# Optimization experiments

Measured on AMD Instinct MI355X. Metric: run time of the kernel, lower is better.

The kernel has to match this reference:

```python
import jax, jax.numpy as jnp
import numpy as np

NUM_HEADS = 16
THETA = 10000.0


def _rope(x, cos, sin):
    # x: [B, H, S, d_k]; cos/sin: [S, d_k//2] broadcast over B, H
    x1 = x[..., 0::2]
    x2 = x[..., 1::2]
    r1 = cos * x1 - sin * x2
    r2 = sin * x1 + cos * x2
    # interleave back: (..., half_d, 2) -> (..., d_k)
    return jnp.stack((r1, r2), axis=-1).reshape(x.shape)


def setup_inputs() -> dict:
    key = jax.random.key(0)
    ks = jax.random.split(key, 5)
    B, S, D = 4, 2048, 1024
    scale = D ** -0.5
    x = jax.random.normal(ks[0], (B, S, D), dtype=jnp.float32)
    wq = jax.random.normal(ks[1], (D, D), dtype=jnp.float32) * scale
    wk = jax.random.normal(ks[2], (D, D), dtype=jnp.float32) * scale
    wv = jax.random.normal(ks[3], (D, D), dtype=jnp.float32) * scale
    wo = jax.random.normal(ks[4], (D, D), dtype=jnp.float32) * scale
    return {"x": x, "wq": wq, "wk": wk, "wv": wv, "wo": wo}


def reference(x, wq, wk, wv, wo):
    B, S, D = x.shape
    H = NUM_HEADS
    dk = D // H

    def proj(w):
        # x @ w.T, split heads -> [B, H, S, dk]
        y = jnp.einsum('bsd,ed->bse', x, w)
        return y.reshape(B, S, H, dk).transpose(0, 2, 1, 3)

    q, k, v = proj(wq), proj(wk), proj(wv)

    # RoPE (interleaved pairs), positions = arange(S)
    inv_freq = THETA ** (-(jnp.arange(0, dk, 2, dtype=jnp.float32) / dk))
    ang = jnp.arange(S, dtype=jnp.float32)[:, None] * inv_freq  # [S, dk//2]
    cos, sin = jnp.cos(ang), jnp.sin(ang)
    q = _rope(q, cos, sin)
    k = _rope(k, cos, sin)

    scores = jnp.einsum('bhqd,bhkd->bhqk', q, k) / jnp.sqrt(jnp.asarray(dk, x.dtype))
    causal = jnp.tril(jnp.ones((S, S), dtype=bool))  # keep self + past
    scores = jnp.where(causal, scores, -jnp.inf)
    p = jax.nn.softmax(scores, axis=-1)
    attn = jnp.einsum('bhqk,bhkd->bhqd', p, v)
    attn = attn.transpose(0, 2, 1, 3).reshape(B, S, D)
    return jnp.einsum('bsd,ed->bse', attn, wo)
```

## Files before the change

### kernel.cpp

```cpp
#include <hip/hip_runtime.h>
#include <hip/hip_bf16.h>
#include <cstdint>
#include <cstddef>

#define Bb 4
#define Ss 2048
#define Dd 1024
#define Hh 16
#define Mm (Bb*Ss)

typedef __bf16 bf16_t;
typedef __bf16 bf16x8 __attribute__((ext_vector_type(8)));
typedef __bf16 bf16x4 __attribute__((ext_vector_type(4)));
typedef float  f32x4  __attribute__((ext_vector_type(4)));
typedef float  f32x16 __attribute__((ext_vector_type(16)));
typedef unsigned int u32x4 __attribute__((ext_vector_type(4)));
typedef unsigned int u32x2 __attribute__((ext_vector_type(2)));

#define MFMA16(a,b,c) __builtin_amdgcn_mfma_f32_16x16x32_bf16(a,b,c,0,0,0)
#define MFMA32(a,b,c) __builtin_amdgcn_mfma_f32_32x32x16_bf16(a,b,c,0,0,0)

#define QSCALE 0.18033688011112042f

static __device__ __forceinline__ float fexp2(float x) {
#if __has_builtin(__builtin_amdgcn_exp2f)
  return __builtin_amdgcn_exp2f(x);
#else
  return exp2f(x);
#endif
}

static __device__ __forceinline__ bf16x8 ld16g(const bf16_t* p) {
  return __builtin_bit_cast(bf16x8, *reinterpret_cast<const u32x4*>(p));
}

static __device__ __forceinline__ void gload_lds16(const bf16_t* g, bf16_t* l) {
  __builtin_amdgcn_global_load_lds(
      (__attribute__((address_space(1))) void*)(g),
      (__attribute__((address_space(3))) void*)(l),
      16, 0, 0);
}

__global__ void cvt_f32_bf16(const float* __restrict__ in, bf16_t* __restrict__ out) {
  int i = (blockIdx.x * blockDim.x + threadIdx.x) * 4;
  float4 f = *reinterpret_cast<const float4*>(in + i);
  out[i + 0] = (bf16_t)f.x;
  out[i + 1] = (bf16_t)f.y;
  out[i + 2] = (bf16_t)f.z;
  out[i + 3] = (bf16_t)f.w;
}

__global__ void cvt_w4(const float* __restrict__ w0, const float* __restrict__ w1,
                       const float* __restrict__ w2, const float* __restrict__ w3,
                       bf16_t* __restrict__ out) {
  int bid = blockIdx.x;
  int seg = bid >> 10, local = bid & 1023;
  const float* w = (seg == 0) ? w0 : (seg == 1) ? w1 : (seg == 2) ? w2 : w3;
  int i = (local * 256 + threadIdx.x) * 4;
  float4 f = *reinterpret_cast<const float4*>(w + i);
  bf16_t* o = out + (size_t)seg * (Dd * Dd) + i;
  o[0] = (bf16_t)f.x; o[1] = (bf16_t)f.y; o[2] = (bf16_t)f.z; o[3] = (bf16_t)f.w;
}

__global__ void rope_tab_k(float2* __restrict__ tab) {
  int idx = blockIdx.x * 256 + threadIdx.x;
  int i = idx & 31, s = idx >> 5;
  float inv_freq = exp2f(-(float)i * (13.2877123795494f / 32.0f));
  float ang = (float)s * inv_freq;
  float sn, cs;
  sincosf(ang, &sn, &cs);
  tab[idx] = make_float2(cs, sn);
}

template <typename OutT>
__global__ __launch_bounds__(256, 3) void gemm_r3(const bf16_t* __restrict__ A,
                                                  const bf16_t* __restrict__ Bm,
                                                  OutT* __restrict__ C0,
                                                  OutT* __restrict__ C1,
                                                  OutT* __restrict__ C2,
                                                  const float2* __restrict__ tab,
                                                  int Kdim) {
  __shared__ bf16_t As[3][128 * 32];
  __shared__ bf16_t Bs[3][128 * 32];
  const int t = threadIdx.x;
  const int lane = t & 63, w = t >> 6;
  const int l15 = lane & 15, lg = lane >> 4;
  const int wr = w >> 1, wc = w & 1;
  const int m0 = blockIdx.x * 128, n0 = blockIdx.y * 128;

  const bf16_t* gA[2];
  const bf16_t* gB[2];
#pragma unroll
  for (int i = 0; i < 2; ++i) {
    int q = i * 256 + t, row = q >> 2, sl = (q & 3) ^ ((row >> 1) & 3);
    gA[i] = A  + (size_t)(m0 + row) * Kdim + sl * 8;
    gB[i] = Bm + (size_t)(n0 + row) * Kdim + sl * 8;
  }
  const int wb = w * 64 * 8;

  auto stage = [&](int slot, int k0) {
#pragma unroll
    for (int i = 0; i < 2; ++i) {
      gload_lds16(gA[i] + k0, &As[slot][i * 2048 + wb]);
      gload_lds16(gB[i] + k0, &Bs[slot][i * 2048 + wb]);
    }
  };

  int aoff[4], boff[4];
#pragma unroll
  for (int i = 0; i < 4; ++i) {
    int row = wr * 64 + i * 16 + l15;
    aoff[i] = row * 32 + ((lg ^ ((row >> 1) & 3)) * 8);
  }
#pragma unroll
  for (int j = 0; j < 4; ++j) {
    int row = wc * 64 + j * 16 + l15;
    boff[j] = row * 32 + ((lg ^ ((row >> 1) & 3)) * 8);
  }

  f32x4 acc[4][4] = {};
  const int KT = Kdim / 32;

  stage(0, 0);
  stage(1, 32);
  for (int j = 0; j < KT; ++j) {
    if (j == KT - 1) {
      asm volatile("s_waitcnt vmcnt(0) lgkmcnt(0)" ::: "memory");
    } else {
      asm volatile("s_waitcnt vmcnt(4) lgkmcnt(0)" ::: "memory");
    }
    __builtin_amdgcn_s_barrier();
    if (j + 2 < KT) stage((j + 2) % 3, (j + 2) * 32);
    const bf16_t* ab = As[j % 3];
    const bf16_t* bb = Bs[j % 3];
    bf16x8 a[4], b[4];
#pragma unroll
    for (int jj = 0; jj < 4; ++jj)
      b[jj] = __builtin_bit_cast(bf16x8,
               *reinterpret_cast<const u32x4*>(bb + boff[jj]));
#pragma unroll
    for (int i = 0; i < 4; ++i)
      a[i] = __builtin_bit_cast(bf16x8,
               *reinterpret_cast<const u32x4*>(ab + aoff[i]));
    __builtin_amdgcn_s_setprio(1);
#pragma unroll
    for (int i = 0; i < 4; ++i)
#pragma unroll
      for (int jj = 0; jj < 4; ++jj)
        acc[i][jj] = MFMA16(a[i], b[jj], acc[i][jj]);
    __builtin_amdgcn_s_setprio(0);
  }

  OutT* Cs = (n0 < 1024) ? C0 : (n0 < 2048 ? C1 : C2);
  const int nb = n0 & 1023;
  const bool doRope = (tab != nullptr) && (n0 < 2048);
  const float qs = (n0 < 1024) ? QSCALE : 1.0f;

  if (doRope) {
#pragma unroll
    for (int i = 0; i < 4; ++i) {
      int rowb = m0 + wr * 64 + i * 16 + lg * 4;
#pragma unroll
      for (int j = 0; j < 4; ++j) {
        int col = nb + wc * 64 + j * 16 + l15;
        int i0 = (col & 63) >> 1;
        const bool ev = !(col & 1);
#pragma unroll
        for (int r = 0; r < 4; ++r) {
          float v = acc[i][j][r];
          float px = __shfl_xor(v, 1);
          int s = (rowb + r) & (Ss - 1);
          float2 f = tab[s * 32 + i0];
          float sn = ev ? -f.y : f.y;
          Cs[(size_t)(rowb + r) * 1024 + col] = (OutT)((f.x * v + sn * px) * qs);
        }
      }
    }
  } else {
#pragma unroll
    for (int i = 0; i < 4; ++i) {
      int rowb = m0 + wr * 64 + i * 16 + lg * 4;
#pragma unroll
      for (int j = 0; j < 4; ++j) {
        int col = nb + wc * 64 + j * 16 + l15;
#pragma unroll
        for (int r = 0; r < 4; ++r)
          Cs[(size_t)(rowb + r) * 1024 + col] = (OutT)acc[i][j][r];
      }
    }
  }
}

__global__ __launch_bounds__(256) void transpose_v(const bf16_t* __restrict__ V,
                                                   bf16_t* __restrict__ Vt) {
  __shared__ bf16_t tile[64][72];
  int bh = blockIdx.y;
  int b = bh >> 4, h = bh & 15;
  int s0 = blockIdx.x * 64;
  int t = threadIdx.x;
  const bf16_t* vbase = V + (size_t)b * Ss * Dd + h * 64;
#pragma unroll
  for (int c = 0; c < 2; ++c) {
    int cf = c * 256 + t;
    int s = cf >> 3, d8 = cf & 7;
    u32x4 v = *reinterpret_cast<const u32x4*>(vbase + (size_t)(s0 + s) * Dd + d8 * 8);
    *reinterpret_cast<u32x4*>(&tile[s][d8 * 8]) = v;
  }
  __syncthreads();
  bf16_t* obase = Vt + (size_t)bh * 64 * Ss;
#pragma unroll
  for (int c = 0; c < 2; ++c) {
    int cf = c * 256 + t;
    int d = cf >> 3, s8 = cf & 7;
    __align__(16) bf16_t tmp[8];
#pragma unroll
    for (int i = 0; i < 8; ++i) tmp[i] = tile[s8 * 8 + i][d];
    *reinterpret_cast<u32x4*>(obase + (size_t)d * Ss + s0 + s8 * 8) =
        *reinterpret_cast<const u32x4*>(tmp);
  }
}

__global__ __launch_bounds__(256, 2) void attn_k(const bf16_t* __restrict__ Q,
                                                 const bf16_t* __restrict__ K,
                                                 const bf16_t* __restrict__ Vt,
                                                 bf16_t* __restrict__ O) {
  __shared__ bf16_t Ks[3][4096];
  __shared__ bf16_t Vs[3][4096];
  const int t = threadIdx.x, lane = t & 63, w = t >> 6;
  const int l31 = lane & 31, hi = lane >> 5, hi8 = hi * 8;
  const int bh = blockIdx.y, b = bh >> 4, h = bh & 15;
  const int bx = blockIdx.x;
  const int i = bx * 4 + w;
  const int q0a = 32 * i, q0b = 2016 - 32 * i;
  const int dtA = q0a >> 6, hfA = (q0a >> 5) & 1;
  const int dtB = q0b >> 6, hfB = (q0b >> 5) & 1;
  const int NT = 32 - 2 * bx;
  const bf16_t* qb = Q + (size_t)b * Ss * Dd + h * 64;
  const bf16_t* kb = K + (size_t)b * Ss * Dd + h * 64;
  const bf16_t* vtb = Vt + (size_t)bh * 64 * Ss;

  const int a_ = l31 >> 2, c_ = l31 & 3;
  const int tau = (a_ >> 1) + 2 * (a_ & 1) + ((a_ & 4) >> 1);
  const int sig = c_ + 4 * tau;

  int kfoff[4];
#pragma unroll
  for (int c = 0; c < 4; ++c) {
    int j = sig >> 1, u = (sig & 1) * 8 + c * 2 + hi;
    kfoff[c] = j * 128 + ((u ^ j) * 8);
  }
  int vfoff[2][2];
#pragma unroll
  for (int db = 0; db < 2; ++db)
#pragma unroll
    for (int ks = 0; ks < 2; ++ks) {
      int d = db * 32 + l31, j = d >> 2, u = (d & 3) * 4 + ks * 2 + hi;
      vfoff[db][ks] = j * 128 + ((u ^ j) * 8);
    }

  const int sj = t >> 4, ss = t & 15, su = ss ^ sj;
  const bf16_t* ksrc0 = kb + (size_t)(2 * sj + (su >> 3)) * Dd + (su & 7) * 8;
  const bf16_t* vsrc0 = vtb + (size_t)(4 * sj + (su >> 2)) * Ss + (su & 3) * 8;

  auto stage = [&](int buf, int kb0) {
    bf16_t* kd = &Ks[buf][w * 512];
    bf16_t* vd = &Vs[buf][w * 512];
    gload_lds16(ksrc0 + (size_t)kb0 * Dd, kd);
    gload_lds16(ksrc0 + (size_t)(kb0 + 32) * Dd, kd + 2048);
    gload_lds16(vsrc0 + kb0, vd);
    gload_lds16(vsrc0 + kb0 + 32, vd + 2048);
  };

  bf16x8 qf[2][4];
#pragma unroll
  for (int c = 0; c < 4; ++c) {
    qf[0][c] = ld16g(qb + (size_t)(q0a + l31) * Dd + c * 16 + hi8);
    qf[1][c] = ld16g(qb + (size_t)(q0b + l31) * Dd + c * 16 + hi8);
  }

  float l_[2] = {0.f, 0.f};
  f32x16 o_[2][2] = {};

  auto chain = [&](int kt, int dt, int hf, bf16x8 (&qc)[4],
                   f32x16& o0, f32x16& o1, float& lc,
                   bf16x8 (&kf)[2][4], bf16x8 (&vf)[2][2][2]) {
    if (kt > dt) return;
    const bool last = (kt == dt);
    const bool do1 = !(last && hf == 0);
    f32x16 s0 = {}, s1 = {};
    __builtin_amdgcn_s_setprio(1);
    s0 = MFMA32(kf[0][0], qc[0], s0);
    s0 = MFMA32(kf[0][1], qc[1], s0);
    s0 = MFMA32(kf[0][2], qc[2], s0);
    s0 = MFMA32(kf[0][3], qc[3], s0);
    if (do1) {
      s1 = MFMA32(kf[1][0], qc[0], s1);
      s1 = MFMA32(kf[1][1], qc[1], s1);
      s1 = MFMA32(kf[1][2], qc[2], s1);
      s1 = MFMA32(kf[1][3], qc[3], s1);
    }
    __builtin_amdgcn_s_setprio(0);
    if (last) {
      if (hf) {
#pragma unroll
        for (int reg = 0; reg < 16; ++reg) {
          const int koff = (reg & 3) + 4 * (reg >> 2) + 8 * ((reg >> 2) >> 1) + hi8;
          s1[reg] = (koff <= l31) ? s1[reg] : -INFINITY;
        }
      } else {
#pragma unroll
        for (int reg = 0; reg < 16; ++reg) {
          const int koff = (reg & 3) + 4 * (reg >> 2) + 8 * ((reg >> 2) >> 1) + hi8;
          s0[reg] = (koff <= l31) ? s0[reg] : -INFINITY;
        }
      }
    }
    float p0[16], p1[16];
#pragma unroll
    for (int r = 0; r < 16; ++r) p0[r] = fexp2(s0[r]);
    bf16x8 pa0, pa1, pb0, pb1;
#pragma unroll
    for (int r = 0; r < 8; ++r) { pa0[r] = (bf16_t)p0[r]; pa1[r] = (bf16_t)p0[r + 8]; }
    if (do1) {
#pragma unroll
      for (int r = 0; r < 16; ++r) p1[r] = fexp2(s1[r]);
#pragma unroll
      for (int r = 0; r < 8; ++r) { pb0[r] = (bf16_t)p1[r]; pb1[r] = (bf16_t)p1[r + 8]; }
#pragma unroll
      for (int r = 0; r < 16; ++r) p0[r] += p1[r];
    }
#pragma unroll
    for (int st2 = 8; st2 > 0; st2 >>= 1)
#pragma unroll
      for (int r = 0; r < st2; ++r) p0[r] += p0[r + st2];
    lc += p0[0];
    __builtin_amdgcn_s_setprio(1);
    o0 = MFMA32(vf[0][0][0], pa0, o0);
    o0 = MFMA32(vf[0][0][1], pa1, o0);
    o1 = MFMA32(vf[0][1][0], pa0, o1);
    o1 = MFMA32(vf[0][1][1], pa1, o1);
    if (do1) {
      o0 = MFMA32(vf[1][0][0], pb0, o0);
      o0 = MFMA32(vf[1][0][1], pb1, o0);
      o1 = MFMA32(vf[1][1][0], pb0, o1);
      o1 = MFMA32(vf[1][1][1], pb1, o1);
    }
    __builtin_amdgcn_s_setprio(0);
  };

  stage(0, 0);
  stage(1, 64);
  for (int j = 0; j < NT; ++j) {
    if (j == NT - 1) {
      asm volatile("s_waitcnt vmcnt(0) lgkmcnt(0)" ::: "memory");
    } else {
      asm volatile("s_waitcnt vmcnt(4) lgkmcnt(0)" ::: "memory");
    }
    __builtin_amdgcn_s_barrier();
    if (j + 2 < NT) stage((j + 2) % 3, (j + 2) * 64);
    const bf16_t* kbuf = &Ks[j % 3][0];
    const bf16_t* vbuf = &Vs[j % 3][0];
    bf16x8 kf[2][4], vf[2][2][2];
#pragma unroll
    for (int st = 0; st < 2; ++st)
#pragma unroll
      for (int c = 0; c < 4; ++c)
        kf[st][c] = __builtin_bit_cast(bf16x8,
            *reinterpret_cast<const u32x4*>(kbuf + st * 2048 + kfoff[c]));
#pragma unroll
    for (int st = 0; st < 2; ++st)
#pragma unroll
      for (int db = 0; db < 2; ++db)
#pragma unroll
        for (int ks = 0; ks < 2; ++ks)
          vf[st][db][ks] = __builtin_bit_cast(bf16x8,
              *reinterpret_cast<const u32x4*>(vbuf + st * 2048 + vfoff[db][ks]));
    chain(j, dtA, hfA, qf[0], o_[0][0], o_[0][1], l_[0], kf, vf);
    chain(j, dtB, hfB, qf[1], o_[1][0], o_[1][1], l_[1], kf, vf);
  }

#pragma unroll
  for (int ch = 0; ch < 2; ++ch) {
    const float ltot = l_[ch] + __shfl_xor(l_[ch], 32);
    const float inv = 1.0f / ltot;
    const size_t rowoff = ((size_t)b * Ss + (ch ? q0b : q0a) + l31) * Dd + h * 64;
#pragma unroll
    for (int db = 0; db < 2; ++db)
#pragma unroll
      for (int tt = 0; tt < 4; ++tt) {
        bf16x4 ov;
#pragma unroll
        for (int c = 0; c < 4; ++c) ov[c] = (bf16_t)(o_[ch][db][4 * tt + c] * inv);
        *reinterpret_cast<u32x2*>(&O[rowoff + db * 32 + 8 * tt + 4 * hi]) =
            __builtin_bit_cast(u32x2, ov);
      }
  }
}

extern "C" void kernel_launch(void* const* d_in, const int* in_sizes, int n_in,
                              void* d_out, int out_size, void* d_ws, size_t ws_size,
                              hipStream_t stream) {
  (void)in_sizes; (void)n_in; (void)out_size; (void)ws_size;
  const float* x  = (const float*)d_in[0];
  const float* wq = (const float*)d_in[1];
  const float* wk = (const float*)d_in[2];
  const float* wv = (const float*)d_in[3];
  const float* wo = (const float*)d_in[4];
  float* out = (float*)d_out;

  char* ws = (char*)d_ws;
  const size_t MB16 = 16u << 20;
  bf16_t* xb   = (bf16_t*)(ws + 0);
  bf16_t* Qb   = (bf16_t*)(ws + 1 * MB16);
  bf16_t* Kb   = (bf16_t*)(ws + 2 * MB16);
  bf16_t* Vb   = (bf16_t*)(ws + 3 * MB16);
  bf16_t* wqkv = (bf16_t*)(ws + 4 * MB16);
  bf16_t* wob  = wqkv + 3u * Dd * Dd;
  float2* tab  = (float2*)(ws + 4 * MB16 + (8u << 20));
  bf16_t* Vt   = xb;
  bf16_t* AOb  = Vb;

  cvt_f32_bf16<<<(Mm * Dd) / 1024, 256, 0, stream>>>(x, xb);
  cvt_w4<<<4096, 256, 0, stream>>>(wq, wk, wv, wo, wqkv);
  rope_tab_k<<<256, 256, 0, stream>>>(tab);

  gemm_r3<bf16_t><<<dim3(Mm / 128, 24), 256, 0, stream>>>(xb, wqkv, Qb, Kb, Vb,
                                                          tab, Dd);

  transpose_v<<<dim3(Ss / 64, Bb * Hh), 256, 0, stream>>>(Vb, Vt);

  attn_k<<<dim3(8, Bb * Hh), 256, 0, stream>>>(Qb, Kb, Vt, AOb);

  gemm_r3<float><<<dim3(Mm / 128, 8), 256, 0, stream>>>(AOb, wob, out, out, out,
                                                        nullptr, Dd);
}
```

Baseline: 176.7 us.

## Fuse prep kernels and remap GEMM/attention blocks for XCD-local L2 reuse

Merges the three preprocessing kernels (x cast, weight cast, RoPE table) into one launch to cut launch overhead. The two GEMMs and the attention kernel now use a linear 1D grid whose index is decoded so that blocks landing on the same XCD (lin & 7) share a column slab of B, or a set of heads. The goal is better per-XCD L2 reuse of weights and K/V. The remapping depends on the round-robin XCD dispatch assumption and on the grid sizes dividing evenly.

```diff
diff --git a/kernel.cpp b/kernel.cpp
--- a/kernel.cpp
+++ b/kernel.cpp
@@ -41,35 +41,34 @@
       16, 0, 0);
 }
 
-__global__ void cvt_f32_bf16(const float* __restrict__ in, bf16_t* __restrict__ out) {
-  int i = (blockIdx.x * blockDim.x + threadIdx.x) * 4;
-  float4 f = *reinterpret_cast<const float4*>(in + i);
-  out[i + 0] = (bf16_t)f.x;
-  out[i + 1] = (bf16_t)f.y;
-  out[i + 2] = (bf16_t)f.z;
-  out[i + 3] = (bf16_t)f.w;
-}
-
-__global__ void cvt_w4(const float* __restrict__ w0, const float* __restrict__ w1,
-                       const float* __restrict__ w2, const float* __restrict__ w3,
-                       bf16_t* __restrict__ out) {
+__global__ void prep_k(const float* __restrict__ x,  const float* __restrict__ wq,
+                       const float* __restrict__ wk, const float* __restrict__ wv,
+                       const float* __restrict__ wo,
+                       bf16_t* __restrict__ xb, bf16_t* __restrict__ wqkv,
+                       float2* __restrict__ tab) {
   int bid = blockIdx.x;
-  int seg = bid >> 10, local = bid & 1023;
-  const float* w = (seg == 0) ? w0 : (seg == 1) ? w1 : (seg == 2) ? w2 : w3;
-  int i = (local * 256 + threadIdx.x) * 4;
-  float4 f = *reinterpret_cast<const float4*>(w + i);
-  bf16_t* o = out + (size_t)seg * (Dd * Dd) + i;
-  o[0] = (bf16_t)f.x; o[1] = (bf16_t)f.y; o[2] = (bf16_t)f.z; o[3] = (bf16_t)f.w;
-}
-
-__global__ void rope_tab_k(float2* __restrict__ tab) {
-  int idx = blockIdx.x * 256 + threadIdx.x;
-  int i = idx & 31, s = idx >> 5;
-  float inv_freq = exp2f(-(float)i * (13.2877123795494f / 32.0f));
-  float ang = (float)s * inv_freq;
-  float sn, cs;
-  sincosf(ang, &sn, &cs);
-  tab[idx] = make_float2(cs, sn);
+  if (bid < 8192) {
+    int i = (bid * 256 + threadIdx.x) * 4;
+    float4 f = *reinterpret_cast<const float4*>(x + i);
+    xb[i + 0] = (bf16_t)f.x; xb[i + 1] = (bf16_t)f.y;
+    xb[i + 2] = (bf16_t)f.z; xb[i + 3] = (bf16_t)f.w;
+  } else if (bid < 12288) {
+    int b2 = bid - 8192;
+    int seg = b2 >> 10, local = b2 & 1023;
+    const float* w = (seg == 0) ? wq : (seg == 1) ? wk : (seg == 2) ? wv : wo;
+    int i = (local * 256 + threadIdx.x) * 4;
+    float4 f = *reinterpret_cast<const float4*>(w + i);
+    bf16_t* o = wqkv + (size_t)seg * (Dd * Dd) + i;
+    o[0] = (bf16_t)f.x; o[1] = (bf16_t)f.y; o[2] = (bf16_t)f.z; o[3] = (bf16_t)f.w;
+  } else {
+    int idx = (bid - 12288) * 256 + threadIdx.x;
+    int i = idx & 31, s = idx >> 5;
+    float inv_freq = exp2f(-(float)i * (13.2877123795494f / 32.0f));
+    float ang = (float)s * inv_freq;
+    float sn, cs;
+    sincosf(ang, &sn, &cs);
+    tab[idx] = make_float2(cs, sn);
+  }
 }
 
 template <typename OutT>
@@ -79,14 +78,19 @@
                                                   OutT* __restrict__ C1,
                                                   OutT* __restrict__ C2,
                                                   const float2* __restrict__ tab,
-                                                  int Kdim) {
+                                                  int Kdim, int ySlab) {
   __shared__ bf16_t As[3][128 * 32];
   __shared__ bf16_t Bs[3][128 * 32];
   const int t = threadIdx.x;
   const int lane = t & 63, w = t >> 6;
   const int l15 = lane & 15, lg = lane >> 4;
   const int wr = w >> 1, wc = w & 1;
-  const int m0 = blockIdx.x * 128, n0 = blockIdx.y * 128;
+
+  const int lin = blockIdx.x;
+  const int xcd = lin & 7, wk_ = lin >> 3;
+  const int xq = wk_ / ySlab, yl = wk_ - xq * ySlab;
+  const int yq = xcd * ySlab + yl;
+  const int m0 = xq * 128, n0 = yq * 128;
 
   const bf16_t* gA[2];
   const bf16_t* gB[2];
@@ -228,8 +232,11 @@
   __shared__ bf16_t Vs[3][4096];
   const int t = threadIdx.x, lane = t & 63, w = t >> 6;
   const int l31 = lane & 31, hi = lane >> 5, hi8 = hi * 8;
-  const int bh = blockIdx.y, b = bh >> 4, h = bh & 15;
-  const int bx = blockIdx.x;
+  const int lin = blockIdx.x;
+  const int xcd = lin & 7, wk_ = lin >> 3;
+  const int bh = xcd * 8 + (wk_ >> 3);
+  const int bx = wk_ & 7;
+  const int b = bh >> 4, h = bh & 15;
   const int i = bx * 4 + w;
   const int q0a = 32 * i, q0b = 2016 - 32 * i;
   const int dtA = q0a >> 6, hfA = (q0a >> 5) & 1;
@@ -420,17 +427,14 @@
   bf16_t* Vt   = xb;
   bf16_t* AOb  = Vb;
 
-  cvt_f32_bf16<<<(Mm * Dd) / 1024, 256, 0, stream>>>(x, xb);
-  cvt_w4<<<4096, 256, 0, stream>>>(wq, wk, wv, wo, wqkv);
-  rope_tab_k<<<256, 256, 0, stream>>>(tab);
-
-  gemm_r3<bf16_t><<<dim3(Mm / 128, 24), 256, 0, stream>>>(xb, wqkv, Qb, Kb, Vb,
-                                                          tab, Dd);
+  prep_k<<<12544, 256, 0, stream>>>(x, wq, wk, wv, wo, xb, wqkv, tab);
+
+  gemm_r3<bf16_t><<<1536, 256, 0, stream>>>(xb, wqkv, Qb, Kb, Vb, tab, Dd, 3);
 
   transpose_v<<<dim3(Ss / 64, Bb * Hh), 256, 0, stream>>>(Vb, Vt);
 
-  attn_k<<<dim3(8, Bb * Hh), 256, 0, stream>>>(Qb, Kb, Vt, AOb);
-
-  gemm_r3<float><<<dim3(Mm / 128, 8), 256, 0, stream>>>(AOb, wob, out, out, out,
-                                                        nullptr, Dd);
-}
+  attn_k<<<512, 256, 0, stream>>>(Qb, Kb, Vt, AOb);
+
+  gemm_r3<float><<<512, 256, 0, stream>>>(AOb, wob, out, out, out,
+                                          nullptr, Dd, 1);
+}
```

Measured after the change: 177.0 us. About the same (+0.1%).
